# Kernel tuning notes

Hardware: AMD Instinct MI355X
Metric: run time of the kernel (lower is better)

The kernel has to match this reference:

```python
import jax, jax.numpy as jnp
import numpy as np

B, S, D_MODEL = 16, 512, 4096
N_HEADS, N_KV_HEADS, HEAD_DIM = 32, 8, 128
ROPE_THETA = 1.0e6
EPS = 1e-6


def setup_inputs() -> dict:
    key = jax.random.key(0)
    ks = jax.random.split(key, 8)
    scale = 0.02
    hidden_states = jax.random.normal(ks[0], (B, S, D_MODEL), dtype=jnp.float32)
    position_ids = jnp.broadcast_to(jnp.arange(S, dtype=jnp.int64 if jax.config.jax_enable_x64 else jnp.int32), (B, S))
    Wq = jax.random.normal(ks[1], (D_MODEL, N_HEADS * HEAD_DIM), dtype=jnp.float32) * scale
    Wk = jax.random.normal(ks[2], (D_MODEL, N_KV_HEADS * HEAD_DIM), dtype=jnp.float32) * scale
    Wv = jax.random.normal(ks[3], (D_MODEL, N_KV_HEADS * HEAD_DIM), dtype=jnp.float32) * scale
    Wo = jax.random.normal(ks[4], (N_HEADS * HEAD_DIM, D_MODEL), dtype=jnp.float32) * scale
    q_norm_w = jnp.ones((HEAD_DIM,), dtype=jnp.float32)
    k_norm_w = jnp.ones((HEAD_DIM,), dtype=jnp.float32)
    return {"hidden_states": hidden_states, "position_ids": position_ids,
            "Wq": Wq, "Wk": Wk, "Wv": Wv, "Wo": Wo,
            "q_norm_w": q_norm_w, "k_norm_w": k_norm_w}


def _rms_norm(x, w):
    # per-head RMSNorm over last dim (head_dim), computed in fp32
    xf = x.astype(jnp.float32)
    var = jnp.mean(xf * xf, axis=-1, keepdims=True)
    return (xf * jax.lax.rsqrt(var + EPS)).astype(x.dtype) * w


def _rope_cos_sin(position_ids, dtype):
    # default rope: inv_freq over half dims, emb = cat(freqs, freqs)
    inv_freq = 1.0 / (ROPE_THETA ** (jnp.arange(0, HEAD_DIM, 2, dtype=jnp.float32) / HEAD_DIM))
    freqs = position_ids.astype(jnp.float32)[:, :, None] * inv_freq[None, None, :]  # [B,S,D/2]
    emb = jnp.concatenate([freqs, freqs], axis=-1)  # [B,S,D]
    return jnp.cos(emb).astype(dtype), jnp.sin(emb).astype(dtype)


def _rotate_half(x):
    x1, x2 = jnp.split(x, 2, axis=-1)
    return jnp.concatenate([-x2, x1], axis=-1)


def reference(hidden_states, position_ids, Wq, Wk, Wv, Wo, q_norm_w, k_norm_w):
    B_, S_, _ = hidden_states.shape
    # QKV projections (no bias in Qwen3)
    q = (hidden_states @ Wq).reshape(B_, S_, N_HEADS, HEAD_DIM)
    k = (hidden_states @ Wk).reshape(B_, S_, N_KV_HEADS, HEAD_DIM)
    v = (hidden_states @ Wv).reshape(B_, S_, N_KV_HEADS, HEAD_DIM)
    # per-head QK RMSNorm
    q = _rms_norm(q, q_norm_w)
    k = _rms_norm(k, k_norm_w)
    # RoPE
    cos, sin = _rope_cos_sin(position_ids, q.dtype)  # [B,S,D]
    cos = cos[:, :, None, :]
    sin = sin[:, :, None, :]
    q = q * cos + _rotate_half(q) * sin
    k = k * cos + _rotate_half(k) * sin
    # GQA attention: expand kv heads to query heads (prefill from position 0;
    # cache write at [:, :S] followed by read of [:, :S] is identity)
    groups = N_HEADS // N_KV_HEADS
    k = jnp.repeat(k, groups, axis=2)  # [B,S,H,D]
    v = jnp.repeat(v, groups, axis=2)
    scale = 1.0 / np.sqrt(HEAD_DIM)
    scores = jnp.einsum('bqhd,bkhd->bhqk', q, k) * scale
    causal = jnp.tril(jnp.ones((S_, S_), dtype=bool))
    scores = jnp.where(causal[None, None], scores, jnp.finfo(scores.dtype).min)
    probs = jax.nn.softmax(scores, axis=-1)
    attn = jnp.einsum('bhqk,bkhd->bqhd', probs, v).reshape(B_, S_, N_HEADS * HEAD_DIM)
    return attn @ Wo
```

## Files before the change

kernel.cpp:

```cpp
#include <hip/hip_runtime.h>

typedef unsigned short u16;
typedef __attribute__((ext_vector_type(4))) unsigned short u16x4;
typedef __attribute__((ext_vector_type(8))) short short8;
typedef __attribute__((ext_vector_type(4))) float f32x4;

#define DEV static __device__ __forceinline__

constexpr int NB   = 16;
constexpr int S    = 512;
constexpr int DM   = 4096;
constexpr int NH   = 32;
constexpr int NKV  = 8;
constexpr int HD   = 128;
constexpr int TOK  = NB * S;
constexpr int NQKV = 6144;
constexpr float ATT_SCALE = 0.08838834764831845f;

DEV u16 f2b(float f) {
  union { float f; unsigned u; } v; v.f = f;
  unsigned r = v.u + 0x7fffu + ((v.u >> 16) & 1u);
  return (u16)(r >> 16);
}
DEV float b2f(u16 u) {
  union { unsigned u; float f; } v; v.u = ((unsigned)u) << 16;
  return v.f;
}
DEV unsigned cvt_pk_bf16(float lo, float hi) {
  unsigned r;
  asm("v_cvt_pk_bf16_f32 %0, %1, %2" : "=v"(r) : "v"(lo), "v"(hi));
  return r;
}
DEV void async16(const void* g, void* l) {
  __builtin_amdgcn_global_load_lds(
      (const __attribute__((address_space(1))) unsigned int*)g,
      (__attribute__((address_space(3))) unsigned int*)l, 16, 0, 0);
}

__global__ __launch_bounds__(256) void k_prep(const float* __restrict__ hs,
                                              const float* __restrict__ Wq,
                                              const float* __restrict__ Wk,
                                              const float* __restrict__ Wv,
                                              const int* __restrict__ pos,
                                              u16* __restrict__ X,
                                              u16* __restrict__ WT,
                                              float2* __restrict__ tab) {
  __shared__ float tile[32][33];
  int blk = blockIdx.x;
  const int tid = threadIdx.x;
  if (blk < 32768) {
    int i = (blk * 256 + tid) * 4;
    const float4 v = *reinterpret_cast<const float4*>(hs + i);
    u16x4 o;
    o[0] = f2b(v.x); o[1] = f2b(v.y); o[2] = f2b(v.z); o[3] = f2b(v.w);
    *reinterpret_cast<u16x4*>(X + i) = o;
    return;
  }
  blk -= 32768;
  if (blk < 2048) {
    int t = blk * 4 + (tid >> 6);
    int j = tid & 63;
    float p = (float)pos[t];
    float inv = expf(-(float)j * 0.21586735246819178f);
    float sv, cv;
    sincosf(p * inv, &sv, &cv);
    tab[t * 64 + j] = make_float2(cv, sv);
    return;
  }
  blk -= 2048;
  const float* src; u16* dst; int ncols, bx, by;
  if (blk < 16384) {
    src = Wq; dst = WT; ncols = 4096; bx = blk & 127; by = blk >> 7;
  } else if (blk < 20480) {
    blk -= 16384;
    src = Wk; dst = WT + (size_t)4096 * 4096; ncols = 1024; bx = blk & 31; by = blk >> 5;
  } else {
    blk -= 20480;
    src = Wv; dst = WT + (size_t)5120 * 4096; ncols = 1024; bx = blk & 31; by = blk >> 5;
  }
  const int tx = tid & 31, ty = tid >> 5;
  const int n0 = bx * 32, k0 = by * 32;
#pragma unroll
  for (int i = 0; i < 32; i += 8)
    tile[ty + i][tx] = src[(size_t)(k0 + ty + i) * ncols + n0 + tx];
  __syncthreads();
#pragma unroll
  for (int i = 0; i < 32; i += 8)
    dst[(size_t)(n0 + ty + i) * 4096 + k0 + tx] = f2b(tile[tx][ty + i]);
}

__global__ __launch_bounds__(256) void k_post(u16* __restrict__ qkv,
                                              const float2* __restrict__ tab,
                                              const float* __restrict__ qw,
                                              const float* __restrict__ kw,
                                              u16* __restrict__ vt,
                                              const float* __restrict__ Wo,
                                              u16* __restrict__ wot) {
  __shared__ float ftile[32][33];
  __shared__ u16 utile[32][33];
  int blk = blockIdx.x;
  const int tid = threadIdx.x;
  if (blk < 10240) {
    int wid  = blk * 4 + (tid >> 6);
    int lane = tid & 63;
    int gr = wid * 8 + (lane >> 3);
    int t  = gr / 40;
    int hh = gr - t * 40;
    bool isq = hh < 32;
    u16* base = qkv + (size_t)t * NQKV + (isq ? hh * 128 : 4096 + (hh - 32) * 128);
    int d0 = (lane & 7) * 8;
    short8 v1 = *reinterpret_cast<const short8*>(base + d0);
    short8 v2 = *reinterpret_cast<const short8*>(base + d0 + 64);
    float x1[8], x2[8];
    float ss = 0.f;
#pragma unroll
    for (int e = 0; e < 8; ++e) {
      x1[e] = b2f((u16)v1[e]);
      x2[e] = b2f((u16)v2[e]);
      ss += x1[e] * x1[e] + x2[e] * x2[e];
    }
    ss += __shfl_xor(ss, 1, 64);
    ss += __shfl_xor(ss, 2, 64);
    ss += __shfl_xor(ss, 4, 64);
    float r = rsqrtf(ss * (1.0f / 128.0f) + 1e-6f);
    const float* w = isq ? qw : kw;
    float sc = isq ? ATT_SCALE : 1.0f;
    short8 o1, o2;
#pragma unroll
    for (int e = 0; e < 8; ++e) {
      float y1 = x1[e] * r * w[d0 + e];
      float y2 = x2[e] * r * w[d0 + e + 64];
      float2 cs = tab[t * 64 + d0 + e];
      o1[e] = (short)f2b((y1 * cs.x - y2 * cs.y) * sc);
      o2[e] = (short)f2b((y2 * cs.x + y1 * cs.y) * sc);
    }
    *reinterpret_cast<short8*>(base + d0)      = o1;
    *reinterpret_cast<short8*>(base + d0 + 64) = o2;
    return;
  }
  blk -= 10240;
  if (blk < 8192) {
    int xx = blk & 3, rest = blk >> 2;
    int yy = rest & 15, bh = rest >> 4;
    int b = bh >> 3, kvh = bh & 7;
    int d0 = xx * 32, s0 = yy * 32;
    int tx = tid & 31, ty = tid >> 5;
#pragma unroll
    for (int i = 0; i < 32; i += 8)
      utile[ty + i][tx] = qkv[(size_t)(b * S + s0 + ty + i) * NQKV + 5120 + kvh * 128 + d0 + tx];
    __syncthreads();
#pragma unroll
    for (int i = 0; i < 32; i += 8)
      vt[((size_t)(bh * 128 + d0 + ty + i)) * S + s0 + tx] = utile[tx][ty + i];
    return;
  }
  blk -= 8192;
  int bx = blk & 127, by = blk >> 7;
  int tx = tid & 31, ty = tid >> 5;
  int n0 = bx * 32, k0 = by * 32;
#pragma unroll
  for (int i = 0; i < 32; i += 8)
    ftile[ty + i][tx] = Wo[(size_t)(k0 + ty + i) * 4096 + n0 + tx];
  __syncthreads();
#pragma unroll
  for (int i = 0; i < 32; i += 8)
    wot[(size_t)(n0 + ty + i) * 4096 + k0 + tx] = f2b(ftile[tx][ty + i]);
}

template <int OUT_BF16>
__global__ __launch_bounds__(512, 2) void k_gemm8(const u16* __restrict__ A,
                                                  const u16* __restrict__ Bm,
                                                  void* __restrict__ Cv,
                                                  int M, int N, int K) {
  __shared__ alignas(16) u16 lds[2][2][256 * 64];
  const int tid  = threadIdx.x;
  const int lane = tid & 63;
  const int wave = tid >> 6;
  const int r16 = lane & 15, h4 = lane >> 4;
  const int wm = (wave >> 2) * 128, wn = (wave & 3) * 64;

  const int nbx = N >> 8;
  const int nby = M >> 8;
  const int nwg = nby * nbx;
  const int cpx = nwg >> 3;
  const int wg  = blockIdx.x;
  const int gidx = (wg & 7) * cpx + (wg >> 3);
  const int by = gidx % nby;
  const int bx = gidx / nby;
  const int m0 = by << 8, n0 = bx << 8;

  const int NKT = K >> 6;
  const int NIT = NKT >> 1;

  f32x4 acc[8][4] = {};
  short8 af[4][2];
  short8 bfr[4][2];

  auto stage = [&](int s) {
    int ts = s >> 2; if (ts > NKT - 1) ts = NKT - 1;
    const int sel  = s & 3;
    const int isB  = sel & 1;
    const int half = (sel == 1 || sel == 2) ? 1 : 0;
    const u16* G = isB ? Bm : A;
    const int base0 = isB ? n0 : m0;
    u16* lb = &lds[ts & 1][isB][0];
    const int k0 = ts << 6;
#pragma unroll
    for (int j = 0; j < 2; ++j) {
      int c = (j << 9) + tid;
      int rl = c >> 3, kcd = c & 7;
      int row = isB ? ((rl & 31) | (half << 5) | ((rl >> 5) << 6))
                    : ((rl & 63) | (half << 6) | ((rl >> 6) << 7));
      int kc = kcd ^ (row & 7);
      async16(G + (size_t)(base0 + row) * K + k0 + (kc << 3),
              lb + row * 64 + (kcd << 3));
    }
  };
  auto ldA = [&](int buf, int mf, int ks) {
    int row = wm + mf * 16 + r16;
    int kc = ((ks << 2) + h4) ^ (r16 & 7);
    return *reinterpret_cast<const short8*>(&lds[buf][0][row * 64 + (kc << 3)]);
  };
  auto ldB = [&](int buf, int nf, int ks) {
    int row = wn + nf * 16 + r16;
    int kc = ((ks << 2) + h4) ^ (r16 & 7);
    return *reinterpret_cast<const short8*>(&lds[buf][1][row * 64 + (kc << 3)]);
  };

#pragma unroll
  for (int s = 0; s < 6; ++s) stage(s);
  asm volatile("s_waitcnt vmcnt(4)" ::: "memory");
  __builtin_amdgcn_s_barrier();

  for (int i = 0; i < NIT; ++i) {
#pragma unroll
    for (int ph = 0; ph < 2; ++ph) {
      const int t = i * 2 + ph;
      const int buf = ph;
#pragma unroll
      for (int mf = 0; mf < 4; ++mf)
#pragma unroll
        for (int ks = 0; ks < 2; ++ks) af[mf][ks] = ldA(buf, mf, ks);
#pragma unroll
      for (int nf = 0; nf < 4; ++nf)
#pragma unroll
        for (int ks = 0; ks < 2; ++ks) bfr[nf][ks] = ldB(buf, nf, ks);
      stage(4 * t + 6);
      stage(4 * t + 7);
      __builtin_amdgcn_s_setprio(1);
#pragma unroll
      for (int mf = 0; mf < 4; ++mf)
#pragma unroll
        for (int nf = 0; nf < 4; ++nf)
#pragma unroll
          for (int ks = 0; ks < 2; ++ks)
            acc[mf][nf] = __builtin_amdgcn_mfma_f32_16x16x32_bf16(
                af[mf][ks], bfr[nf][ks], acc[mf][nf], 0, 0, 0);
      __builtin_amdgcn_s_setprio(0);
      __builtin_amdgcn_s_barrier();
#pragma unroll
      for (int mf = 0; mf < 4; ++mf)
#pragma unroll
        for (int ks = 0; ks < 2; ++ks) af[mf][ks] = ldA(buf, 4 + mf, ks);
      stage(4 * t + 8);
      stage(4 * t + 9);
      __builtin_amdgcn_s_setprio(1);
#pragma unroll
      for (int mf = 0; mf < 4; ++mf)
#pragma unroll
        for (int nf = 0; nf < 4; ++nf)
#pragma unroll
          for (int ks = 0; ks < 2; ++ks)
            acc[4 + mf][nf] = __builtin_amdgcn_mfma_f32_16x16x32_bf16(
                af[mf][ks], bfr[nf][ks], acc[4 + mf][nf], 0, 0, 0);
      __builtin_amdgcn_s_setprio(0);
      asm volatile("s_waitcnt vmcnt(4)" ::: "memory");
      __builtin_amdgcn_s_barrier();
    }
  }

  if (OUT_BF16) {
    u16* C = (u16*)Cv;
#pragma unroll
    for (int mf = 0; mf < 8; ++mf)
#pragma unroll
      for (int nf = 0; nf < 4; ++nf)
#pragma unroll
        for (int r = 0; r < 4; ++r) {
          size_t row = m0 + wm + mf * 16 + h4 * 4 + r;
          size_t col = n0 + wn + nf * 16 + r16;
          C[row * N + col] = f2b(acc[mf][nf][r]);
        }
  } else {
    float* C = (float*)Cv;
#pragma unroll
    for (int mf = 0; mf < 8; ++mf)
#pragma unroll
      for (int nf = 0; nf < 4; ++nf)
#pragma unroll
        for (int r = 0; r < 4; ++r) {
          size_t row = m0 + wm + mf * 16 + h4 * 4 + r;
          size_t col = n0 + wn + nf * 16 + r16;
          C[row * N + col] = acc[mf][nf][r];
        }
  }
}

__global__ __launch_bounds__(256) void k_attn(const u16* __restrict__ qkv,
                                              const u16* __restrict__ vt,
                                              u16* __restrict__ out) {
  __shared__ alignas(16) u16 Klds[2][64 * 128];
  __shared__ alignas(16) u16 Vlds[2][128 * 64];
  __shared__ alignas(16) u16 Plds[4][2][16 * 64];
  const int kvh = blockIdx.x, b = blockIdx.y;
  const int qt = 15 - blockIdx.z;
  const int tid = threadIdx.x, lane = tid & 63, wave = tid >> 6;
  const int r16 = lane & 15, h4 = lane >> 4;
  const int h = kvh * 4 + wave;
  const int qr0 = qt * 32;

  auto stageKV = [&](int t, int buf) {
    const int k0 = t << 6;
    const u16* kg = qkv + (size_t)(b * S + k0) * NQKV + 4096 + kvh * 128;
#pragma unroll
    for (int it = 0; it < 4; ++it) {
      int c = tid + (it << 8);
      int key = c >> 4, c8 = c & 15;
      int jc = c8 ^ (key & 7);
      async16(kg + (size_t)key * NQKV + jc * 8, &Klds[buf][c * 8]);
    }
    const u16* vg = vt + (size_t)(b * 8 + kvh) * 128 * S + k0;
#pragma unroll
    for (int it = 0; it < 4; ++it) {
      int c = tid + (it << 8);
      int d = c >> 3, c8 = c & 7;
      int jc = c8 ^ (d & 7);
      async16(vg + (size_t)d * S + jc * 8, &Vlds[buf][c * 8]);
    }
  };
  auto ldK = [&](int buf, int f, int s4) {
    int key = f * 16 + r16;
    int idx = (key * 128 + s4 * 32 + h4 * 8) ^ ((key & 7) << 3);
    return *reinterpret_cast<const short8*>(&Klds[buf][idx]);
  };
  auto ldV = [&](int buf, int df, int ks) {
    int d = df * 16 + r16;
    int idx = (d * 64 + ks * 32 + h4 * 8) ^ ((d & 7) << 3);
    return *reinterpret_cast<const short8*>(&Vlds[buf][idx]);
  };

  short8 qf[2][4];
#pragma unroll
  for (int rf = 0; rf < 2; ++rf) {
    const u16* qrow = qkv + (size_t)(b * S + qr0 + rf * 16 + r16) * NQKV + h * 128 + h4 * 8;
#pragma unroll
    for (int s4 = 0; s4 < 4; ++s4)
      qf[rf][s4] = *reinterpret_cast<const short8*>(qrow + s4 * 32);
  }

  float mrow[2] = {-INFINITY, -INFINITY};
  float lrow[2] = {0.f, 0.f};
  f32x4 o[2][8] = {};

  const int ntiles = (qt >> 1) + 1;
  stageKV(0, 0);
  __syncthreads();

  for (int t = 0; t < ntiles; ++t) {
    const int buf = t & 1;
    if (t + 1 < ntiles) stageKV(t + 1, buf ^ 1);
    const int k0 = t << 6;
    const bool diag = (t == ntiles - 1);
    int fa0 = 4, fa1 = 4;
    if (diag) {
      fa0 = ((qr0 - k0 + 15) >> 4) + 1; if (fa0 > 4) fa0 = 4;
      fa1 = ((qr0 - k0 + 31) >> 4) + 1; if (fa1 > 4) fa1 = 4;
    }
    const int ks_act = (fa1 + 1) >> 1;

    f32x4 sacc[2][4] = {};
    __builtin_amdgcn_s_setprio(1);
#pragma unroll
    for (int f = 0; f < 4; ++f) {
      if (f < fa1) {
        short8 kf[4];
#pragma unroll
        for (int s4 = 0; s4 < 4; ++s4) kf[s4] = ldK(buf, f, s4);
#pragma unroll
        for (int s4 = 0; s4 < 4; ++s4) {
          if (f < fa0)
            sacc[0][f] = __builtin_amdgcn_mfma_f32_16x16x32_bf16(kf[s4], qf[0][s4], sacc[0][f], 0, 0, 0);
          sacc[1][f] = __builtin_amdgcn_mfma_f32_16x16x32_bf16(kf[s4], qf[1][s4], sacc[1][f], 0, 0, 0);
        }
      }
    }
    __builtin_amdgcn_s_setprio(0);
    if (diag) {
#pragma unroll
      for (int rf = 0; rf < 2; ++rf)
#pragma unroll
        for (int f = 0; f < 4; ++f)
#pragma unroll
          for (int r = 0; r < 4; ++r) {
            int key = k0 + f * 16 + h4 * 4 + r;
            int row = qr0 + rf * 16 + r16;
            if (key > row) sacc[rf][f][r] = -1e30f;
          }
    }
#pragma unroll
    for (int rf = 0; rf < 2; ++rf) {
      float mx = sacc[rf][0][0];
#pragma unroll
      for (int f = 0; f < 4; ++f)
#pragma unroll
        for (int r = 0; r < 4; ++r) mx = fmaxf(mx, sacc[rf][f][r]);
      mx = fmaxf(mx, __shfl_xor(mx, 16, 64));
      mx = fmaxf(mx, __shfl_xor(mx, 32, 64));
      if (!__all(mx - mrow[rf] <= 8.0f)) {
        float mn = fmaxf(mrow[rf], mx);
        float fac = __expf(mrow[rf] - mn);
        mrow[rf] = mn;
        lrow[rf] *= fac;
#pragma unroll
        for (int df = 0; df < 8; ++df)
#pragma unroll
          for (int r = 0; r < 4; ++r) o[rf][df][r] *= fac;
      }
      float psum = 0.f;
#pragma unroll
      for (int f = 0; f < 4; ++f)
#pragma unroll
        for (int r = 0; r < 4; ++r) {
          float p = __expf(sacc[rf][f][r] - mrow[rf]);
          sacc[rf][f][r] = p;
          psum += p;
        }
      psum += __shfl_xor(psum, 16, 64);
      psum += __shfl_xor(psum, 32, 64);
      lrow[rf] += psum;
    }

#pragma unroll
    for (int rf = 0; rf < 2; ++rf)
#pragma unroll
      for (int f = 0; f < 4; ++f) {
        uint2 w;
        w.x = cvt_pk_bf16(sacc[rf][f][0], sacc[rf][f][1]);
        w.y = cvt_pk_bf16(sacc[rf][f][2], sacc[rf][f][3]);
        int idx = r16 * 64 + ((f * 16 + h4 * 4) ^ ((r16 & 7) << 3));
        *reinterpret_cast<uint2*>(&Plds[wave][rf][idx]) = w;
      }
    short8 pf[2][2];
#pragma unroll
    for (int rf = 0; rf < 2; ++rf)
#pragma unroll
      for (int ks = 0; ks < 2; ++ks)
        if (ks < ks_act) {
          int idx = r16 * 64 + ((ks * 32 + h4 * 8) ^ ((r16 & 7) << 3));
          pf[rf][ks] = *reinterpret_cast<const short8*>(&Plds[wave][rf][idx]);
        }
    __builtin_amdgcn_s_setprio(1);
#pragma unroll
    for (int df = 0; df < 8; ++df)
#pragma unroll
      for (int ks = 0; ks < 2; ++ks)
        if (ks < ks_act) {
          short8 vf = ldV(buf, df, ks);
#pragma unroll
          for (int rf = 0; rf < 2; ++rf)
            o[rf][df] = __builtin_amdgcn_mfma_f32_16x16x32_bf16(vf, pf[rf][ks], o[rf][df], 0, 0, 0);
        }
    __builtin_amdgcn_s_setprio(0);
    __syncthreads();
  }

#pragma unroll
  for (int rf = 0; rf < 2; ++rf) {
    float rinv = 1.0f / lrow[rf];
    int row = qr0 + rf * 16 + r16;
    u16* orow = out + (size_t)(b * S + row) * 4096 + h * 128;
#pragma unroll
    for (int df = 0; df < 8; ++df) {
      unsigned p0 = cvt_pk_bf16(o[rf][df][0] * rinv, o[rf][df][1] * rinv);
      unsigned p1 = cvt_pk_bf16(o[rf][df][2] * rinv, o[rf][df][3] * rinv);
      uint2 pk; pk.x = p0; pk.y = p1;
      *reinterpret_cast<uint2*>(orow + df * 16 + h4 * 4) = pk;
    }
  }
}

extern "C" void kernel_launch(void* const* d_in, const int* in_sizes, int n_in,
                              void* d_out, int out_size, void* d_ws, size_t ws_size,
                              hipStream_t stream) {
  const float* hs  = (const float*)d_in[0];
  const int*   pos = (const int*)d_in[1];
  const float* Wq  = (const float*)d_in[2];
  const float* Wk  = (const float*)d_in[3];
  const float* Wv  = (const float*)d_in[4];
  const float* Wo  = (const float*)d_in[5];
  const float* qnw = (const float*)d_in[6];
  const float* knw = (const float*)d_in[7];

  char* ws = (char*)d_ws;
  u16*   X    = (u16*)(ws);
  u16*   WT   = (u16*)(ws + 67108864);
  u16*   QKV  = (u16*)(ws + 117440512);
  u16*   VT   = (u16*)(ws + 218103808);
  float2* TAB = (float2*)(ws + 234881024);
  u16*   ATTN = X;
  u16*   WOT  = WT;

  k_prep<<<59392, 256, 0, stream>>>(hs, Wq, Wk, Wv, pos, X, WT, TAB);
  k_gemm8<1><<<(8192 / 256) * (6144 / 256), 512, 0, stream>>>(X, WT, QKV, 8192, 6144, 4096);
  k_post<<<34816, 256, 0, stream>>>(QKV, TAB, qnw, knw, VT, Wo, WOT);
  k_attn<<<dim3(8, 16, 16), 256, 0, stream>>>(QKV, VT, ATTN);
  k_gemm8<0><<<(8192 / 256) * (4096 / 256), 512, 0, stream>>>(ATTN, WOT, d_out, 8192, 4096, 4096);
}
```

Baseline: 800.5 us.

## Move Wo transpose into attention launch and remap attention grid per XCD

The Wo transpose-to-bf16 blocks move out of the post-projection kernel and become extra trailing workgroups of the attention kernel, reusing the K LDS buffer as the staging tile. They can then fill compute units left idle during the uneven causal-attention tail. The attention grid is flattened to 1D and remapped so that every query tile of a given (batch, kv-head) pair lands on the same XCD. That aims to improve L2 reuse of K/V. The cost is extra index arithmetic and transpose blocks that may compete with attention for bandwidth.

```diff
diff --git a/kernel.cpp b/kernel.cpp
--- a/kernel.cpp
+++ b/kernel.cpp
@@ -93,10 +93,7 @@
                                               const float2* __restrict__ tab,
                                               const float* __restrict__ qw,
                                               const float* __restrict__ kw,
-                                              u16* __restrict__ vt,
-                                              const float* __restrict__ Wo,
-                                              u16* __restrict__ wot) {
-  __shared__ float ftile[32][33];
+                                              u16* __restrict__ vt) {
   __shared__ u16 utile[32][33];
   int blk = blockIdx.x;
   const int tid = threadIdx.x;
@@ -139,32 +136,18 @@
     return;
   }
   blk -= 10240;
-  if (blk < 8192) {
-    int xx = blk & 3, rest = blk >> 2;
-    int yy = rest & 15, bh = rest >> 4;
-    int b = bh >> 3, kvh = bh & 7;
-    int d0 = xx * 32, s0 = yy * 32;
-    int tx = tid & 31, ty = tid >> 5;
-#pragma unroll
-    for (int i = 0; i < 32; i += 8)
-      utile[ty + i][tx] = qkv[(size_t)(b * S + s0 + ty + i) * NQKV + 5120 + kvh * 128 + d0 + tx];
-    __syncthreads();
-#pragma unroll
-    for (int i = 0; i < 32; i += 8)
-      vt[((size_t)(bh * 128 + d0 + ty + i)) * S + s0 + tx] = utile[tx][ty + i];
-    return;
-  }
-  blk -= 8192;
-  int bx = blk & 127, by = blk >> 7;
+  int xx = blk & 3, rest = blk >> 2;
+  int yy = rest & 15, bh = rest >> 4;
+  int b = bh >> 3, kvh = bh & 7;
+  int d0 = xx * 32, s0 = yy * 32;
   int tx = tid & 31, ty = tid >> 5;
-  int n0 = bx * 32, k0 = by * 32;
 #pragma unroll
   for (int i = 0; i < 32; i += 8)
-    ftile[ty + i][tx] = Wo[(size_t)(k0 + ty + i) * 4096 + n0 + tx];
+    utile[ty + i][tx] = qkv[(size_t)(b * S + s0 + ty + i) * NQKV + 5120 + kvh * 128 + d0 + tx];
   __syncthreads();
 #pragma unroll
   for (int i = 0; i < 32; i += 8)
-    wot[(size_t)(n0 + ty + i) * 4096 + k0 + tx] = f2b(ftile[tx][ty + i]);
+    vt[((size_t)(bh * 128 + d0 + ty + i)) * S + s0 + tx] = utile[tx][ty + i];
 }
 
 template <int OUT_BF16>
@@ -308,13 +291,35 @@
 
 __global__ __launch_bounds__(256) void k_attn(const u16* __restrict__ qkv,
                                               const u16* __restrict__ vt,
-                                              u16* __restrict__ out) {
+                                              u16* __restrict__ out,
+                                              const float* __restrict__ Wo,
+                                              u16* __restrict__ wot) {
   __shared__ alignas(16) u16 Klds[2][64 * 128];
   __shared__ alignas(16) u16 Vlds[2][128 * 64];
   __shared__ alignas(16) u16 Plds[4][2][16 * 64];
-  const int kvh = blockIdx.x, b = blockIdx.y;
-  const int qt = 15 - blockIdx.z;
-  const int tid = threadIdx.x, lane = tid & 63, wave = tid >> 6;
+  const int tid = threadIdx.x;
+  const int wg = blockIdx.x;
+  if (wg >= 2048) {
+    float* ftile = reinterpret_cast<float*>(&Klds[0][0]);
+    int idx = wg - 2048;
+    int bx = idx & 127, by = idx >> 7;
+    int tx = tid & 31, ty = tid >> 5;
+    int n0 = bx * 32, k0 = by * 32;
+#pragma unroll
+    for (int i = 0; i < 32; i += 8)
+      ftile[(ty + i) * 33 + tx] = Wo[(size_t)(k0 + ty + i) * 4096 + n0 + tx];
+    __syncthreads();
+#pragma unroll
+    for (int i = 0; i < 32; i += 8)
+      wot[(size_t)(n0 + ty + i) * 4096 + k0 + tx] = f2b(ftile[tx * 33 + ty + i]);
+    return;
+  }
+  const int xcd = wg & 7;
+  const int p   = wg >> 3;
+  const int qt  = 15 - (p >> 4);
+  const int family = xcd * 16 + (p & 15);
+  const int kvh = family & 7, b = family >> 3;
+  const int lane = tid & 63, wave = tid >> 6;
   const int r16 = lane & 15, h4 = lane >> 4;
   const int h = kvh * 4 + wave;
   const int qr0 = qt * 32;
@@ -431,9 +436,9 @@
       for (int f = 0; f < 4; ++f)
 #pragma unroll
         for (int r = 0; r < 4; ++r) {
-          float p = __expf(sacc[rf][f][r] - mrow[rf]);
-          sacc[rf][f][r] = p;
-          psum += p;
+          float pv = __expf(sacc[rf][f][r] - mrow[rf]);
+          sacc[rf][f][r] = pv;
+          psum += pv;
         }
       psum += __shfl_xor(psum, 16, 64);
       psum += __shfl_xor(psum, 32, 64);
@@ -512,7 +517,7 @@
 
   k_prep<<<59392, 256, 0, stream>>>(hs, Wq, Wk, Wv, pos, X, WT, TAB);
   k_gemm8<1><<<(8192 / 256) * (6144 / 256), 512, 0, stream>>>(X, WT, QKV, 8192, 6144, 4096);
-  k_post<<<34816, 256, 0, stream>>>(QKV, TAB, qnw, knw, VT, Wo, WOT);
-  k_attn<<<dim3(8, 16, 16), 256, 0, stream>>>(QKV, VT, ATTN);
+  k_post<<<18432, 256, 0, stream>>>(QKV, TAB, qnw, knw, VT);
+  k_attn<<<18432, 256, 0, stream>>>(QKV, VT, ATTN, Wo, WOT);
   k_gemm8<0><<<(8192 / 256) * (4096 / 256), 512, 0, stream>>>(ATTN, WOT, d_out, 8192, 4096, 4096);
 }
```

Measured after the change: 830.0 us. +3.7%, slower.
